# Kernel optimization log

Measured on AMD Instinct MI355X. Metric: run time of the kernel, lower is better.

The kernel has to match this reference:

```python
import jax, jax.numpy as jnp
import numpy as np

# ---------------- Chu-Liu-Edmonds MST decode (faithful numpy port) ----------------

def _find_cycle(parents, length, current_nodes):
    added = [False] * length
    added[0] = True
    cycle = set()
    has_cycle = False
    for i in range(1, length):
        if has_cycle:
            break
        if added[i] or not current_nodes[i]:
            continue
        this_cycle = {i}
        added[i] = True
        has_cycle = True
        next_node = i
        while parents[next_node] not in this_cycle:
            next_node = parents[next_node]
            if added[next_node]:
                has_cycle = False
                break
            added[next_node] = True
            this_cycle.add(next_node)
        if has_cycle:
            original = next_node
            cycle.add(original)
            next_node = parents[original]
            while next_node != original:
                cycle.add(next_node)
                next_node = parents[next_node]
            break
    return has_cycle, list(cycle)


def chu_liu_edmonds(length, score_matrix, current_nodes, final_edges, old_input, old_output, representatives):
    parents = [-1]
    for node1 in range(1, length):
        parents.append(0)
        if current_nodes[node1]:
            max_score = score_matrix[0, node1]
            for node2 in range(1, length):
                if node2 == node1 or not current_nodes[node2]:
                    continue
                new_score = score_matrix[node2, node1]
                if new_score > max_score:
                    max_score = new_score
                    parents[node1] = node2
    has_cycle, cycle = _find_cycle(parents, length, current_nodes)
    if not has_cycle:
        final_edges[0] = -1
        for node in range(1, length):
            if not current_nodes[node]:
                continue
            parent = old_input[parents[node], node]
            child = old_output[parents[node], node]
            final_edges[child] = parent
        return
    cycle_weight = 0.0
    for node in cycle:
        cycle_weight += score_matrix[parents[node], node]
    cycle_representative = cycle[0]
    for node in range(length):
        if not current_nodes[node] or node in cycle:
            continue
        in_edge_weight = float('-inf')
        in_edge = -1
        out_edge_weight = float('-inf')
        out_edge = -1
        for node_in_cycle in cycle:
            if score_matrix[node_in_cycle, node] > in_edge_weight:
                in_edge_weight = score_matrix[node_in_cycle, node]
                in_edge = node_in_cycle
            score = cycle_weight + score_matrix[node, node_in_cycle] - score_matrix[parents[node_in_cycle], node_in_cycle]
            if score > out_edge_weight:
                out_edge_weight = score
                out_edge = node_in_cycle
        score_matrix[cycle_representative, node] = in_edge_weight
        old_input[cycle_representative, node] = old_input[in_edge, node]
        old_output[cycle_representative, node] = old_output[in_edge, node]
        score_matrix[node, cycle_representative] = out_edge_weight
        old_output[node, cycle_representative] = old_output[node, out_edge]
        old_input[node, cycle_representative] = old_input[node, out_edge]
    considered = []
    for i, node_in_cycle in enumerate(cycle):
        considered.append(set())
        if i > 0:
            current_nodes[node_in_cycle] = False
        for node in representatives[node_in_cycle]:
            considered[i].add(node)
            if i > 0:
                representatives[cycle_representative].add(node)
    chu_liu_edmonds(length, score_matrix, current_nodes, final_edges, old_input, old_output, representatives)
    found = False
    key_node = -1
    for i, node in enumerate(cycle):
        for cycle_rep in considered[i]:
            if cycle_rep in final_edges:
                key_node = node
                found = True
                break
        if found:
            break
    previous = parents[key_node]
    while previous != key_node:
        child = old_output[parents[previous], previous]
        parent = old_input[parents[previous], previous]
        final_edges[child] = parent
        previous = parents[previous]


def decode_mst(energy, length):
    # energy: numpy [num_labels, T, T]
    max_length = energy.shape[-1]
    energy = energy[:, :length, :length]
    label_id_matrix = energy.argmax(axis=0)
    score_matrix = np.array(energy.max(axis=0), copy=True)
    old_input = np.zeros([length, length], dtype=np.int32)
    old_output = np.zeros([length, length], dtype=np.int32)
    current_nodes = [True] * length
    representatives = []
    for node1 in range(length):
        score_matrix[node1, node1] = 0.0
        representatives.append({node1})
        for node2 in range(node1 + 1, length):
            old_input[node1, node2] = node1
            old_output[node1, node2] = node2
            old_input[node2, node1] = node2
            old_output[node2, node1] = node1
    final_edges = {}
    chu_liu_edmonds(length, score_matrix, current_nodes, final_edges, old_input, old_output, representatives)
    heads = np.zeros([max_length], np.int32)
    head_type = np.ones([max_length], np.int32)
    for child, parent in final_edges.items():
        heads[child] = parent
        head_type[child] = label_id_matrix[parent, child]
    return heads, head_type


# ---------------- biaffine scoring (jax) ----------------

@jax.jit
def _energy(encoded_text, W_head_arc, b_head_arc, W_dep_arc, b_dep_arc, U_arc,
            W_head_lab, b_head_lab, W_dep_lab, b_dep_lab, U_lab):
    h_arc = jax.nn.elu(encoded_text @ W_head_arc + b_head_arc)   # [B,T,A]
    d_arc = jax.nn.elu(encoded_text @ W_dep_arc + b_dep_arc)     # [B,T,A]
    arc_scores = jnp.einsum('bia,ac,bjc->bij', h_arc, U_arc, d_arc)  # head i -> dep j
    h_lab = jax.nn.elu(encoded_text @ W_head_lab + b_head_lab)   # [B,T,R]
    d_lab = jax.nn.elu(encoded_text @ W_dep_lab + b_dep_lab)     # [B,T,R]
    lab_scores = jnp.einsum('bir,lrs,bjs->blij', h_lab, U_lab, d_lab)  # [B,L,T,T]
    norm_arc = jax.nn.log_softmax(arc_scores, axis=1)   # normalize over heads
    norm_lab = jax.nn.log_softmax(lab_scores, axis=1)   # normalize over labels
    return jnp.exp(norm_arc[:, None, :, :] + norm_lab)  # [B,L,T,T] edge energies


def setup_inputs() -> dict:
    key = jax.random.key(0)
    ks = jax.random.split(key, 8)
    B, T, D, A, R, L = 32, 128, 768, 512, 128, 50
    s = 0.02
    return {
        'encoded_text': jax.random.normal(ks[0], (B, T, D), jnp.float32),
        'W_head_arc': jax.random.normal(ks[1], (D, A), jnp.float32) * s,
        'b_head_arc': jnp.zeros((A,), jnp.float32),
        'W_dep_arc': jax.random.normal(ks[2], (D, A), jnp.float32) * s,
        'b_dep_arc': jnp.zeros((A,), jnp.float32),
        'U_arc': jax.random.normal(ks[3], (A, A), jnp.float32) * s,
        'W_head_lab': jax.random.normal(ks[4], (D, R), jnp.float32) * s,
        'b_head_lab': jnp.zeros((R,), jnp.float32),
        'W_dep_lab': jax.random.normal(ks[5], (D, R), jnp.float32) * s,
        'b_dep_lab': jnp.zeros((R,), jnp.float32),
        'U_lab': jax.random.normal(ks[6], (L, R, R), jnp.float32) * s,
        'mask': jnp.ones((B, T), jnp.bool_),
    }


def reference(encoded_text, W_head_arc, b_head_arc, W_dep_arc, b_dep_arc, U_arc,
              W_head_lab, b_head_lab, W_dep_lab, b_dep_lab, U_lab, mask):
    energy = _energy(encoded_text, W_head_arc, b_head_arc, W_dep_arc, b_dep_arc, U_arc,
                     W_head_lab, b_head_lab, W_dep_lab, b_dep_lab, U_lab)
    lengths = np.asarray(mask.sum(-1))
    energy_np = np.asarray(energy)
    heads, tags = [], []
    # per-example Chu-Liu-Edmonds decode (inherently sequential, as in the original)
    for i in range(energy_np.shape[0]):
        h, t = decode_mst(energy_np[i], int(lengths[i]))
        heads.append(h)
        tags.append(t)
    return energy, jnp.asarray(np.stack(heads)), jnp.asarray(np.stack(tags))
```

## Files before the change

### kernel.cpp

```cpp
#include <hip/hip_runtime.h>
#include <math.h>

#define B_ 32
#define T_ 128
#define D_ 768
#define A_ 512
#define R_ 128
#define L_ 50

__global__ __launch_bounds__(256)
void proj_gemm_k(const float* __restrict__ X,
                 const float* __restrict__ Wha, const float* __restrict__ bha,
                 const float* __restrict__ Wda, const float* __restrict__ bda,
                 const float* __restrict__ Whl, const float* __restrict__ bhl,
                 const float* __restrict__ Wdl, const float* __restrict__ bdl,
                 float* __restrict__ HA, float* __restrict__ DA,
                 float* __restrict__ HL, float* __restrict__ DL)
{
    __shared__ float As[16][68];
    __shared__ float Bs[16][132];
    const int bx = blockIdx.x;
    const float *W, *bias; float* C; int ld, ncol;
    if (bx < 4)      { W = Wha; bias = bha; C = HA; ld = 512; ncol = bx * 128; }
    else if (bx < 8) { W = Wda; bias = bda; C = DA; ld = 512; ncol = (bx - 4) * 128; }
    else if (bx == 8){ W = Whl; bias = bhl; C = HL; ld = 128; ncol = 0; }
    else             { W = Wdl; bias = bdl; C = DL; ld = 128; ncol = 0; }
    const int m0 = blockIdx.y * 64;
    const int tid = threadIdx.x;
    const int tx = tid & 15, ry = tid >> 4;
    float acc[4][8] = {};
    for (int k0 = 0; k0 < 768; k0 += 16) {
        {
            int row = tid >> 2, kb = (tid & 3) * 4;
            float4 a = *(const float4*)&X[(size_t)(m0 + row) * 768 + k0 + kb];
            As[kb + 0][row] = a.x; As[kb + 1][row] = a.y;
            As[kb + 2][row] = a.z; As[kb + 3][row] = a.w;
        }
        {
            int kk = tid >> 4, c0 = (tid & 15) * 4;
            const float* Bp = &W[(size_t)(k0 + kk) * ld + ncol + c0];
            *(float4*)&Bs[kk][c0] = *(const float4*)&Bp[0];
            *(float4*)&Bs[kk][c0 + 64] = *(const float4*)&Bp[64];
        }
        __syncthreads();
#pragma unroll
        for (int kk = 0; kk < 16; ++kk) {
            float4 a4 = *(const float4*)&As[kk][ry * 4];
            float4 b0 = *(const float4*)&Bs[kk][tx * 4];
            float4 b1 = *(const float4*)&Bs[kk][tx * 4 + 64];
            float av[4] = { a4.x, a4.y, a4.z, a4.w };
            float bv[8] = { b0.x, b0.y, b0.z, b0.w, b1.x, b1.y, b1.z, b1.w };
#pragma unroll
            for (int i = 0; i < 4; ++i)
#pragma unroll
                for (int j = 0; j < 8; ++j)
                    acc[i][j] += av[i] * bv[j];
        }
        __syncthreads();
    }
    float bv0[8];
    {
        float4 q0 = *(const float4*)&bias[ncol + tx * 4];
        float4 q1 = *(const float4*)&bias[ncol + tx * 4 + 64];
        bv0[0] = q0.x; bv0[1] = q0.y; bv0[2] = q0.z; bv0[3] = q0.w;
        bv0[4] = q1.x; bv0[5] = q1.y; bv0[6] = q1.z; bv0[7] = q1.w;
    }
#pragma unroll
    for (int i = 0; i < 4; ++i) {
        int m = m0 + ry * 4 + i;
        size_t base = (size_t)m * ld + ncol;
        float o[8];
#pragma unroll
        for (int j = 0; j < 8; ++j) {
            float v = acc[i][j] + bv0[j];
            o[j] = v > 0.0f ? v : expm1f(v);
        }
        float4 s0 = { o[0], o[1], o[2], o[3] };
        float4 s1 = { o[4], o[5], o[6], o[7] };
        *(float4*)&C[base + tx * 4] = s0;
        *(float4*)&C[base + tx * 4 + 64] = s1;
    }
}

__global__ __launch_bounds__(256)
void gemm_k(const float* __restrict__ A, const float* __restrict__ B,
            const float* __restrict__ bias, float* __restrict__ C,
            int K, int lda, int ldb, int ldc,
            long long sA, long long sB, long long sC, long long c_outer, int flags)
{
    __shared__ float As[16][68];
    __shared__ float Bs[16][132];
    A += (size_t)blockIdx.z * sA;
    B += (size_t)blockIdx.z * sB;
    C += (size_t)blockIdx.z * sC;
    const int m0 = blockIdx.y * 64, n0 = blockIdx.x * 128;
    const int tid = threadIdx.x;
    const int tx = tid & 15, ry = tid >> 4;
    float acc[4][8] = {};
    for (int k0 = 0; k0 < K; k0 += 16) {
        {
            int row = tid >> 2, kb = (tid & 3) * 4;
            float4 a = *(const float4*)&A[(size_t)(m0 + row) * lda + k0 + kb];
            As[kb + 0][row] = a.x; As[kb + 1][row] = a.y;
            As[kb + 2][row] = a.z; As[kb + 3][row] = a.w;
        }
        if (!(flags & 4)) {
            int kk = tid >> 4, c0 = (tid & 15) * 4;
            const float* Bp = &B[(size_t)(k0 + kk) * ldb + n0 + c0];
            *(float4*)&Bs[kk][c0] = *(const float4*)&Bp[0];
            *(float4*)&Bs[kk][c0 + 64] = *(const float4*)&Bp[64];
        } else {
            int col = tid >> 1, kb = (tid & 1) * 8;
            const float* Bp = &B[(size_t)(n0 + col) * ldb + k0 + kb];
            float4 b0 = *(const float4*)&Bp[0];
            float4 b1 = *(const float4*)&Bp[4];
            Bs[kb + 0][col] = b0.x; Bs[kb + 1][col] = b0.y;
            Bs[kb + 2][col] = b0.z; Bs[kb + 3][col] = b0.w;
            Bs[kb + 4][col] = b1.x; Bs[kb + 5][col] = b1.y;
            Bs[kb + 6][col] = b1.z; Bs[kb + 7][col] = b1.w;
        }
        __syncthreads();
#pragma unroll
        for (int kk = 0; kk < 16; ++kk) {
            float4 a4 = *(const float4*)&As[kk][ry * 4];
            float4 b0 = *(const float4*)&Bs[kk][tx * 4];
            float4 b1 = *(const float4*)&Bs[kk][tx * 4 + 64];
            float av[4] = { a4.x, a4.y, a4.z, a4.w };
            float bv[8] = { b0.x, b0.y, b0.z, b0.w, b1.x, b1.y, b1.z, b1.w };
#pragma unroll
            for (int i = 0; i < 4; ++i)
#pragma unroll
                for (int j = 0; j < 8; ++j)
                    acc[i][j] += av[i] * bv[j];
        }
        __syncthreads();
    }
    float bv0[8] = {};
    if (flags & 1) {
        float4 q0 = *(const float4*)&bias[n0 + tx * 4];
        float4 q1 = *(const float4*)&bias[n0 + tx * 4 + 64];
        bv0[0] = q0.x; bv0[1] = q0.y; bv0[2] = q0.z; bv0[3] = q0.w;
        bv0[4] = q1.x; bv0[5] = q1.y; bv0[6] = q1.z; bv0[7] = q1.w;
    }
#pragma unroll
    for (int i = 0; i < 4; ++i) {
        int m = m0 + ry * 4 + i;
        size_t base = (size_t)(m >> 7) * c_outer + (size_t)(m & 127) * ldc + n0;
        float o[8];
#pragma unroll
        for (int j = 0; j < 8; ++j) {
            float v = acc[i][j] + bv0[j];
            if (flags & 2) v = v > 0.0f ? v : expm1f(v);
            o[j] = v;
        }
        float4 s0 = { o[0], o[1], o[2], o[3] };
        float4 s1 = { o[4], o[5], o[6], o[7] };
        *(float4*)&C[base + tx * 4] = s0;
        *(float4*)&C[base + tx * 4 + 64] = s1;
    }
}

__global__ __launch_bounds__(256)
void transpose_k(const float* __restrict__ in, float* __restrict__ out)
{
    __shared__ float tile[32][33];
    int b = blockIdx.z;
    int bx = blockIdx.x, by = blockIdx.y;
    int tx = threadIdx.x, ty = threadIdx.y;
    const float* src = in + (size_t)b * T_ * R_;
    float* dst = out + (size_t)b * T_ * R_;
#pragma unroll
    for (int r = 0; r < 4; ++r)
        tile[ty + 8 * r][tx] = src[(size_t)(by * 32 + ty + 8 * r) * 128 + bx * 32 + tx];
    __syncthreads();
#pragma unroll
    for (int r = 0; r < 4; ++r)
        dst[(size_t)(bx * 32 + ty + 8 * r) * 128 + by * 32 + tx] = tile[tx][ty + 8 * r];
}

__global__ __launch_bounds__(128)
void arc_logsoftmax_k(float* __restrict__ arc)
{
    int b = blockIdx.x, j = threadIdx.x;
    float* base = arc + (size_t)b * T_ * T_ + j;
    float m = -INFINITY;
    for (int i = 0; i < T_; ++i) m = fmaxf(m, base[(size_t)i * T_]);
    float s = 0.0f;
    for (int i = 0; i < T_; ++i) s += expf(base[(size_t)i * T_] - m);
    float ls = m + logf(s);
    for (int i = 0; i < T_; ++i) base[(size_t)i * T_] -= ls;
}

__global__ __launch_bounds__(256)
void lab_inplace_k(float* __restrict__ E, const float* __restrict__ dlt)
{
    __shared__ __align__(16) float As[T_ * R_];
    int l = blockIdx.x, b = blockIdx.y;
    float* base = E + ((size_t)b * L_ + l) * T_ * T_;
    int tid = threadIdx.x;
#pragma unroll
    for (int it = 0; it < 16; ++it) {
        int idx = (it * 256 + tid) * 4;
        *(float4*)&As[idx] = *(const float4*)&base[idx];
    }
    __syncthreads();
    int tx = tid & 15, ty = tid >> 4;
    int j0 = tx * 8, i0 = ty * 8;
    const float* dl = dlt + (size_t)b * T_ * R_;
    float acc[8][8] = {};
    for (int s0 = 0; s0 < R_; s0 += 4) {
        float a[8][4], bb[4][8];
#pragma unroll
        for (int ii = 0; ii < 8; ++ii) {
            float4 v = *(const float4*)&As[(i0 + ii) * R_ + s0];
            a[ii][0] = v.x; a[ii][1] = v.y; a[ii][2] = v.z; a[ii][3] = v.w;
        }
#pragma unroll
        for (int ss = 0; ss < 4; ++ss) {
            float4 x = *(const float4*)&dl[(size_t)(s0 + ss) * T_ + j0];
            float4 y = *(const float4*)&dl[(size_t)(s0 + ss) * T_ + j0 + 4];
            bb[ss][0] = x.x; bb[ss][1] = x.y; bb[ss][2] = x.z; bb[ss][3] = x.w;
            bb[ss][4] = y.x; bb[ss][5] = y.y; bb[ss][6] = y.z; bb[ss][7] = y.w;
        }
#pragma unroll
        for (int ii = 0; ii < 8; ++ii)
#pragma unroll
            for (int jj = 0; jj < 8; ++jj)
#pragma unroll
                for (int ss = 0; ss < 4; ++ss)
                    acc[ii][jj] += a[ii][ss] * bb[ss][jj];
    }
#pragma unroll
    for (int ii = 0; ii < 8; ++ii) {
        float4 o0 = { acc[ii][0], acc[ii][1], acc[ii][2], acc[ii][3] };
        float4 o1 = { acc[ii][4], acc[ii][5], acc[ii][6], acc[ii][7] };
        *(float4*)&base[(size_t)(i0 + ii) * T_ + j0] = o0;
        *(float4*)&base[(size_t)(i0 + ii) * T_ + j0 + 4] = o1;
    }
}

__global__ __launch_bounds__(256)
void energy_combine_k(float* __restrict__ E, const float* __restrict__ narc,
                      float* __restrict__ score_g, unsigned char* __restrict__ labmax_g)
{
    int g = blockIdx.x * 256 + threadIdx.x;
    int b = g >> 14;
    int ij = g & 16383;
    float* base = E + (size_t)b * L_ * T_ * T_ + ij;
    float v[L_];
    float m = -INFINITY;
    int am = 0;
#pragma unroll
    for (int l = 0; l < L_; ++l) {
        v[l] = base[(size_t)l * T_ * T_];
        if (v[l] > m) { m = v[l]; am = l; }
    }
    float s = 0.0f;
#pragma unroll
    for (int l = 0; l < L_; ++l) s += expf(v[l] - m);
    float ls = m + logf(s);
    float na = narc[(size_t)b * T_ * T_ + ij];
#pragma unroll
    for (int l = 0; l < L_; ++l) base[(size_t)l * T_ * T_] = expf(na + v[l] - ls);
    int i = ij >> 7, j = ij & 127;
    score_g[(size_t)b * 16384 + ij] = (i == j) ? 0.0f : expf(na + m - ls);
    labmax_g[(size_t)b * 16384 + ij] = (unsigned char)am;
}

__global__ __launch_bounds__(256)
void mst_k(const float* __restrict__ score_g, const unsigned char* __restrict__ labmax_g,
           float* __restrict__ heads, float* __restrict__ tags,
           unsigned char* __restrict__ pst_ws, unsigned char* __restrict__ tst_ws,
           unsigned char* __restrict__ cst_ws)
{
    int b = blockIdx.x, t = threadIdx.x;
    __shared__ float score[128 * 128];
    __shared__ unsigned char oin[128 * 128];
    __shared__ unsigned char oout[128 * 128];
    __shared__ int parents[128];
    __shared__ int fe[128];
    __shared__ float pmx[128];
    __shared__ int pp[128];
    __shared__ float sub[128];
    __shared__ unsigned char curr[128], cyc[128], cycidx[128], oncyc[128], pstrow[128];
    __shared__ int key_sh;

    volatile float* vscore = score;
    volatile int* vpar = parents;
    volatile int* vfe = fe;
    volatile unsigned char* vcurr = curr;
    volatile unsigned char* vcyc = cyc;
    volatile unsigned char* vcycidx = cycidx;
    volatile unsigned char* voncyc = oncyc;
    volatile unsigned char* voin = oin;
    volatile unsigned char* voout = oout;
    volatile unsigned char* vpstrow = pstrow;
    volatile float* vsub = sub;

    unsigned char* pst = pst_ws + (size_t)b * 16384;
    unsigned char* tst = tst_ws + (size_t)b * 16384;
    unsigned char* cst = cst_ws + (size_t)b * 16384;

    {
        const float4* src = (const float4*)(score_g + (size_t)b * 16384);
#pragma unroll
        for (int r = 0; r < 16; ++r)
            ((float4*)score)[r * 256 + t] = src[r * 256 + t];
    }
    {
        int row = t >> 1, half = t & 1;
        unsigned int tv = (unsigned int)row * 0x01010101u;
        unsigned int* oinw = (unsigned int*)&oin[row * 128];
        unsigned int* ooutw = (unsigned int*)&oout[row * 128];
#pragma unroll
        for (int w = 0; w < 16; ++w) {
            int idx = half * 16 + w;
            oinw[idx] = tv;
            ooutw[idx] = 0x03020100u + 0x04040404u * (unsigned int)idx;
        }
    }
    if (t < 128) { fe[t] = -2; curr[t] = 1; }
    __syncthreads();
    if (t < 128) {
        score[t * 128 + t] = -INFINITY;
        oin[t * 129] = 0; oout[t * 129] = 0;
    }
    __syncthreads();
    float mxl = 0.0f; int pl = 0;
    if (t >= 128) {
        int col = t - 128;
        float mx = -INFINITY; int pu = 64;
        if (col != 0) {
            mx = score[64 * 128 + col];
#pragma unroll 16
            for (int n2 = 65; n2 < 128; ++n2) {
                float sc = score[n2 * 128 + col];
                if (sc > mx) { mx = sc; pu = n2; }
            }
        }
        pmx[col] = mx; pp[col] = pu;
    } else if (t != 0) {
        mxl = score[t]; pl = 0;
#pragma unroll 16
        for (int n2 = 1; n2 < 64; ++n2) {
            float sc = score[n2 * 128 + t];
            if (sc > mxl) { mxl = sc; pl = n2; }
        }
    }
    __syncthreads();
    if (t == 0) parents[0] = -1;
    else if (t < 128) parents[t] = (pmx[t] > mxl) ? pp[t] : pl;
    __syncthreads();

    if (t < 64) {
        const int n0 = t, n1 = t + 64;
        int p0 = vpar[n0], p1 = vpar[n1];
        int c0 = 1, c1 = 1;
        int r0 = n0, r1 = n1;
        int lev = 0;
        for (;;) {
            int a0 = (n0 == 0 || !c0) ? 0 : p0;
            int a1 = (!c1) ? 0 : p1;
            int m0 = n0, m1 = n1;
#pragma unroll
            for (int s = 0; s < 7; ++s) {
                int src0 = a0 & 63, sel0 = a0 & 64;
                int src1 = a1 & 63, sel1 = a1 & 64;
                int g00 = __shfl(a0, src0, 64);
                int g01 = __shfl(a1, src0, 64);
                int h00 = __shfl(m0, src0, 64);
                int h01 = __shfl(m1, src0, 64);
                int g10 = __shfl(a0, src1, 64);
                int g11 = __shfl(a1, src1, 64);
                int h10 = __shfl(m0, src1, 64);
                int h11 = __shfl(m1, src1, 64);
                int na0 = sel0 ? g01 : g00;
                int nm0 = sel0 ? h01 : h00;
                int na1 = sel1 ? g11 : g10;
                int nm1 = sel1 ? h11 : h10;
                m0 = nm0 < m0 ? nm0 : m0;
                m1 = nm1 < m1 ? nm1 : m1;
                a0 = na0; a1 = na1;
            }
            int pred0 = (n0 >= 1) && c0 && (a0 != 0);
            int pred1 = c1 && (a1 != 0);
            unsigned long long bal0 = __ballot(pred0);
            unsigned long long bal1 = __ballot(pred1);
            if (bal0 == 0ull && bal1 == 0ull) {
                if (n0 == 0) vfe[0] = -1;
                else if (c0) {
                    int pa = voin[p0 * 128 + n0];
                    int ch = voout[p0 * 128 + n0];
                    vfe[ch] = pa;
                }
                if (c1) {
                    int pa = voin[p1 * 128 + n1];
                    int ch = voout[p1 * 128 + n1];
                    vfe[ch] = pa;
                }
                __threadfence_block();
                break;
            }
            voncyc[n0] = 0; voncyc[n1] = 0;
            __threadfence_block();
            if (pred0) voncyc[a0] = 1;
            if (pred1) voncyc[a1] = 1;
            __threadfence_block();
            int onc0 = voncyc[n0], onc1 = voncyc[n1];
            int cand0 = onc0 ? n0 : 255;
            int cand1 = onc1 ? n1 : 255;
            int cand = cand1 < cand0 ? cand1 : cand0;
#pragma unroll
            for (int off = 32; off >= 1; off >>= 1) {
                int oc = __shfl_xor(cand, off, 64);
                cand = oc < cand ? oc : cand;
            }
            const int rep = cand;
            int member0 = onc0 && (m0 == rep);
            int member1 = onc1 && (m1 == rep);
            unsigned long long mb0 = __ballot(member0);
            unsigned long long mb1 = __ballot(member1);
            int clen = __popcll(mb0) + __popcll(mb1);
            int rank0 = (int)__popcll(mb0 & ((1ull << n0) - 1ull));
            int rank1 = (int)__popcll(mb0) + (int)__popcll(mb1 & ((1ull << t) - 1ull));
            float s0m = 0.0f, s1m = 0.0f;
            if (member0) s0m = vscore[p0 * 128 + n0];
            if (member1) s1m = vscore[p1 * 128 + n1];
            float cw = s0m + s1m;
#pragma unroll
            for (int off = 32; off >= 1; off >>= 1)
                cw += __shfl_xor(cw, off, 64);
            vcycidx[n0] = member0 ? (unsigned char)rank0 : (unsigned char)0xFF;
            vcycidx[n1] = member1 ? (unsigned char)rank1 : (unsigned char)0xFF;
            if (member0) { vcyc[rank0] = (unsigned char)n0; vsub[rank0] = s0m;
                           cst[lev * 128 + rank0] = (unsigned char)n0; }
            if (member1) { vcyc[rank1] = (unsigned char)n1; vsub[rank1] = s1m;
                           cst[lev * 128 + rank1] = (unsigned char)n1; }
            __threadfence_block();
            pst[lev * 128 + n0] = (unsigned char)p0;
            pst[lev * 128 + n1] = (unsigned char)p1;
            int tg0 = vcycidx[r0], tg1 = vcycidx[r1];
            tst[lev * 128 + n0] = (unsigned char)tg0;
            tst[lev * 128 + n1] = (unsigned char)tg1;
#pragma unroll
            for (int half = 0; half < 2; ++half) {
                int n = half ? n1 : n0;
                int cc = half ? c1 : c0;
                int mem = half ? member1 : member0;
                if (cc && !mem) {
                    float inw = -INFINITY, outw = -INFINITY;
                    int ine = 0, oute = 0;
                    for (int i = 0; i < clen; ++i) {
                        int nic = (int)vcyc[i];
                        float sb = vsub[i];
                        float si = vscore[nic * 128 + n];
                        if (si > inw) { inw = si; ine = nic; }
                        float so = cw + vscore[n * 128 + nic] - sb;
                        if (so > outw) { outw = so; oute = nic; }
                    }
                    vscore[rep * 128 + n] = inw;
                    voin[rep * 128 + n] = voin[ine * 128 + n];
                    voout[rep * 128 + n] = voout[ine * 128 + n];
                    vscore[n * 128 + rep] = outw;
                    voout[n * 128 + rep] = voout[n * 128 + oute];
                    voin[n * 128 + rep] = voin[n * 128 + oute];
                }
            }
            __threadfence_block();
            if (member0 && n0 != rep) { c0 = 0; vcurr[n0] = 0; }
            if (member1 && n1 != rep) { c1 = 0; vcurr[n1] = 0; }
            if (tg0 != 0xFF) r0 = rep;
            if (tg1 != 0xFF) r1 = rep;
            if (c0 && n0 != 0 && n0 != rep && vcycidx[p0] != 0xFF) p0 = rep;
            if (c1 && n1 != rep && vcycidx[p1] != 0xFF) p1 = rep;
            {
                float cv0 = c0 ? vscore[n0 * 128 + rep] : -INFINITY;
                float cv1 = c1 ? vscore[n1 * 128 + rep] : -INFINITY;
                float bv; int bi;
                if (cv1 > cv0) { bv = cv1; bi = n1; } else { bv = cv0; bi = n0; }
#pragma unroll
                for (int off = 32; off >= 1; off >>= 1) {
                    float ov = __shfl_xor(bv, off, 64);
                    int oi = __shfl_xor(bi, off, 64);
                    if (ov > bv || (ov == bv && oi < bi)) { bv = ov; bi = oi; }
                }
                if (n0 == rep) p0 = bi;
                if (n1 == rep) p1 = bi;
            }
            vpar[n0] = p0; vpar[n1] = p1;
            __threadfence_block();
            ++lev;
        }
        for (int l2 = lev - 1; l2 >= 0; --l2) {
            int q0 = pst[l2 * 128 + n0], q1 = pst[l2 * 128 + n1];
            vpstrow[n0] = (unsigned char)q0;
            vpstrow[n1] = (unsigned char)q1;
            int tg0 = tst[l2 * 128 + n0], tg1 = tst[l2 * 128 + n1];
            __threadfence_block();
            if (tg0 != 0xFF && vfe[n0] != -2) *(volatile int*)&key_sh = (int)cst[l2 * 128 + tg0];
            if (tg1 != 0xFF && vfe[n1] != -2) *(volatile int*)&key_sh = (int)cst[l2 * 128 + tg1];
            __threadfence_block();
            if (t == 0) {
                int key = *(volatile int*)&key_sh;
                int prev = (int)vpstrow[key];
                int guard = 0;
                while (prev != key && guard++ < 200) {
                    int pp2 = (int)vpstrow[prev];
                    int ch = (int)voout[pp2 * 128 + prev];
                    int pa = (int)voin[pp2 * 128 + prev];
                    vfe[ch] = pa;
                    prev = pp2;
                }
            }
            __threadfence_block();
        }
    }
    __syncthreads();

    if (t < 128) {
        int f = fe[t];
        float h, ht;
        if (f != -2) {
            h = (float)f;
            int prow = (f < 0) ? 127 : f;
            ht = (float)(int)labmax_g[(size_t)b * 16384 + prow * 128 + t];
        } else { h = 0.0f; ht = 1.0f; }
        heads[b * 128 + t] = h;
        tags[b * 128 + t] = ht;
    }
}

extern "C" void kernel_launch(void* const* d_in, const int* in_sizes, int n_in,
                              void* d_out, int out_size, void* d_ws, size_t ws_size,
                              hipStream_t stream)
{
    const float* X   = (const float*)d_in[0];
    const float* Wha = (const float*)d_in[1];
    const float* bha = (const float*)d_in[2];
    const float* Wda = (const float*)d_in[3];
    const float* bda = (const float*)d_in[4];
    const float* Ua  = (const float*)d_in[5];
    const float* Whl = (const float*)d_in[6];
    const float* bhl = (const float*)d_in[7];
    const float* Wdl = (const float*)d_in[8];
    const float* bdl = (const float*)d_in[9];
    const float* Ul  = (const float*)d_in[10];

    char* ws = (char*)d_ws;
    float* HA    = (float*)(ws + (size_t)0);
    float* DA    = (float*)(ws + ((size_t)8 << 20));
    float* TA    = (float*)(ws + ((size_t)16 << 20));
    float* HL    = (float*)(ws + ((size_t)24 << 20));
    float* DL    = (float*)(ws + ((size_t)26 << 20));
    float* DLt   = (float*)(ws + ((size_t)28 << 20));
    float* ARC   = (float*)(ws + ((size_t)30 << 20));
    float* SCORE = (float*)(ws + ((size_t)32 << 20));
    unsigned char* LABMAX = (unsigned char*)(ws + ((size_t)34 << 20));
    unsigned char* PST  = LABMAX + (size_t)32 * 16384;
    unsigned char* TST  = PST  + (size_t)32 * 16384;
    unsigned char* CST  = TST  + (size_t)32 * 16384;

    float* E     = (float*)d_out;
    float* heads = E + (size_t)B_ * L_ * T_ * T_;
    float* tags  = heads + (size_t)B_ * T_;

    dim3 thr(256);
    proj_gemm_k<<<dim3(10, 64), thr, 0, stream>>>(X, Wha, bha, Wda, bda, Whl, bhl, Wdl, bdl,
                                                  HA, DA, HL, DL);
    gemm_k<<<dim3(4, 64, 1), thr, 0, stream>>>(HA, Ua, nullptr, TA, 512, 512, 512, 512, 0, 0, 0, (long long)128 * 512, 0);
    transpose_k<<<dim3(4, 4, 32), dim3(32, 8), 0, stream>>>(DL, DLt);
    gemm_k<<<dim3(1, 2, 32), thr, 0, stream>>>(TA, DA, nullptr, ARC, 512, 512, 512, 128, 65536, 65536, 16384, 0, 4);
    arc_logsoftmax_k<<<32, 128, 0, stream>>>(ARC);
    gemm_k<<<dim3(1, 64, 50), thr, 0, stream>>>(HL, Ul, nullptr, E, 128, 128, 128, 128, 0, 16384, 16384, (long long)50 * 16384, 0);
    lab_inplace_k<<<dim3(50, 32), thr, 0, stream>>>(E, DLt);
    energy_combine_k<<<2048, 256, 0, stream>>>(E, ARC, SCORE, LABMAX);
    mst_k<<<32, 256, 0, stream>>>(SCORE, LABMAX, heads, tags, PST, TST, CST);
}
```

Baseline: 1.032 ms.

## Move MST contraction history to LDS and streamline cycle detection in wavefront

Moves the per-level contraction history arrays (parent, tag and cycle tables) out of global workspace and into shared memory. The pointer-jumping loop now packs parent and minimum into one word, halving the shuffles per round, and runs only as many rounds as the active node count needs. Cycle marking uses epoch-stamped bytes with a ballot instead of a clear pass and a shuffle reduction, and membership checks read ballot masks instead of a shared index array. Shared memory rises by 48 KB per block, and the cycle-weight sum is now a serial loop over the cycle length.

```diff
diff --git a/kernel.cpp b/kernel.cpp
--- a/kernel.cpp
+++ b/kernel.cpp
@@ -269,37 +269,34 @@
 
 __global__ __launch_bounds__(256)
 void mst_k(const float* __restrict__ score_g, const unsigned char* __restrict__ labmax_g,
-           float* __restrict__ heads, float* __restrict__ tags,
-           unsigned char* __restrict__ pst_ws, unsigned char* __restrict__ tst_ws,
-           unsigned char* __restrict__ cst_ws)
+           float* __restrict__ heads, float* __restrict__ tags)
 {
     int b = blockIdx.x, t = threadIdx.x;
     __shared__ float score[128 * 128];
     __shared__ unsigned char oin[128 * 128];
     __shared__ unsigned char oout[128 * 128];
+    __shared__ unsigned char pstL[128 * 128];
+    __shared__ unsigned char tstL[128 * 128];
+    __shared__ unsigned char cstL[128 * 128];
     __shared__ int parents[128];
     __shared__ int fe[128];
     __shared__ float pmx[128];
     __shared__ int pp[128];
     __shared__ float sub[128];
-    __shared__ unsigned char curr[128], cyc[128], cycidx[128], oncyc[128], pstrow[128];
-    __shared__ int key_sh;
+    __shared__ unsigned char cyc[128], oncyc[128], pstrow[128];
 
     volatile float* vscore = score;
     volatile int* vpar = parents;
     volatile int* vfe = fe;
-    volatile unsigned char* vcurr = curr;
     volatile unsigned char* vcyc = cyc;
-    volatile unsigned char* vcycidx = cycidx;
     volatile unsigned char* voncyc = oncyc;
     volatile unsigned char* voin = oin;
     volatile unsigned char* voout = oout;
     volatile unsigned char* vpstrow = pstrow;
     volatile float* vsub = sub;
-
-    unsigned char* pst = pst_ws + (size_t)b * 16384;
-    unsigned char* tst = tst_ws + (size_t)b * 16384;
-    unsigned char* cst = cst_ws + (size_t)b * 16384;
+    volatile unsigned char* vcst = cstL;
+    volatile unsigned char* vpst = pstL;
+    volatile unsigned char* vtst = tstL;
 
     {
         const float4* src = (const float4*)(score_g + (size_t)b * 16384);
@@ -319,7 +316,7 @@
             ooutw[idx] = 0x03020100u + 0x04040404u * (unsigned int)idx;
         }
     }
-    if (t < 128) { fe[t] = -2; curr[t] = 1; }
+    if (t < 128) { fe[t] = -2; oncyc[t] = 0; }
     __syncthreads();
     if (t < 128) {
         score[t * 128 + t] = -INFINITY;
@@ -358,29 +355,24 @@
         int c0 = 1, c1 = 1;
         int r0 = n0, r1 = n1;
         int lev = 0;
+        int nact = 128;
         for (;;) {
+            int rounds = 32 - __clz(nact - 1);
             int a0 = (n0 == 0 || !c0) ? 0 : p0;
             int a1 = (!c1) ? 0 : p1;
             int m0 = n0, m1 = n1;
-#pragma unroll
-            for (int s = 0; s < 7; ++s) {
-                int src0 = a0 & 63, sel0 = a0 & 64;
-                int src1 = a1 & 63, sel1 = a1 & 64;
-                int g00 = __shfl(a0, src0, 64);
-                int g01 = __shfl(a1, src0, 64);
-                int h00 = __shfl(m0, src0, 64);
-                int h01 = __shfl(m1, src0, 64);
-                int g10 = __shfl(a0, src1, 64);
-                int g11 = __shfl(a1, src1, 64);
-                int h10 = __shfl(m0, src1, 64);
-                int h11 = __shfl(m1, src1, 64);
-                int na0 = sel0 ? g01 : g00;
-                int nm0 = sel0 ? h01 : h00;
-                int na1 = sel1 ? g11 : g10;
-                int nm1 = sel1 ? h11 : h10;
-                m0 = nm0 < m0 ? nm0 : m0;
-                m1 = nm1 < m1 ? nm1 : m1;
-                a0 = na0; a1 = na1;
+            for (int s = 0; s < rounds; ++s) {
+                int pk0 = (a0 << 7) | m0;
+                int pk1 = (a1 << 7) | m1;
+                int s0l = a0 & 63, s1l = a1 & 63;
+                int q00 = __shfl(pk0, s0l, 64);
+                int q01 = __shfl(pk1, s0l, 64);
+                int q10 = __shfl(pk0, s1l, 64);
+                int q11 = __shfl(pk1, s1l, 64);
+                int g0 = (a0 & 64) ? q01 : q00;
+                int g1 = (a1 & 64) ? q11 : q10;
+                a0 = g0 >> 7; int gm0 = g0 & 127; m0 = gm0 < m0 ? gm0 : m0;
+                a1 = g1 >> 7; int gm1 = g1 & 127; m1 = gm1 < m1 ? gm1 : m1;
             }
             int pred0 = (n0 >= 1) && c0 && (a0 != 0);
             int pred1 = c1 && (a1 != 0);
@@ -401,47 +393,44 @@
                 __threadfence_block();
                 break;
             }
-            voncyc[n0] = 0; voncyc[n1] = 0;
+            unsigned char ep = (unsigned char)(lev + 1);
+            if (pred0) voncyc[a0] = ep;
+            if (pred1) voncyc[a1] = ep;
             __threadfence_block();
-            if (pred0) voncyc[a0] = 1;
-            if (pred1) voncyc[a1] = 1;
-            __threadfence_block();
-            int onc0 = voncyc[n0], onc1 = voncyc[n1];
-            int cand0 = onc0 ? n0 : 255;
-            int cand1 = onc1 ? n1 : 255;
-            int cand = cand1 < cand0 ? cand1 : cand0;
-#pragma unroll
-            for (int off = 32; off >= 1; off >>= 1) {
-                int oc = __shfl_xor(cand, off, 64);
-                cand = oc < cand ? oc : cand;
-            }
-            const int rep = cand;
+            int onc0 = (voncyc[n0] == ep);
+            int onc1 = (voncyc[n1] == ep);
+            unsigned long long ob0 = __ballot(onc0);
+            unsigned long long ob1 = __ballot(onc1);
+            const int rep = ob0 ? ((int)__ffsll((long long)ob0) - 1)
+                                : (64 + (int)__ffsll((long long)ob1) - 1);
             int member0 = onc0 && (m0 == rep);
             int member1 = onc1 && (m1 == rep);
             unsigned long long mb0 = __ballot(member0);
             unsigned long long mb1 = __ballot(member1);
-            int clen = __popcll(mb0) + __popcll(mb1);
+            int clen = (int)__popcll(mb0) + (int)__popcll(mb1);
             int rank0 = (int)__popcll(mb0 & ((1ull << n0) - 1ull));
-            int rank1 = (int)__popcll(mb0) + (int)__popcll(mb1 & ((1ull << t) - 1ull));
-            float s0m = 0.0f, s1m = 0.0f;
-            if (member0) s0m = vscore[p0 * 128 + n0];
-            if (member1) s1m = vscore[p1 * 128 + n1];
-            float cw = s0m + s1m;
-#pragma unroll
-            for (int off = 32; off >= 1; off >>= 1)
-                cw += __shfl_xor(cw, off, 64);
-            vcycidx[n0] = member0 ? (unsigned char)rank0 : (unsigned char)0xFF;
-            vcycidx[n1] = member1 ? (unsigned char)rank1 : (unsigned char)0xFF;
+            int rank1 = (int)__popcll(mb0) + (int)__popcll(mb1 & ((1ull << n0) - 1ull));
+            float s0m = member0 ? vscore[p0 * 128 + n0] : 0.0f;
+            float s1m = member1 ? vscore[p1 * 128 + n1] : 0.0f;
             if (member0) { vcyc[rank0] = (unsigned char)n0; vsub[rank0] = s0m;
-                           cst[lev * 128 + rank0] = (unsigned char)n0; }
+                           vcst[lev * 128 + rank0] = (unsigned char)n0; }
             if (member1) { vcyc[rank1] = (unsigned char)n1; vsub[rank1] = s1m;
-                           cst[lev * 128 + rank1] = (unsigned char)n1; }
+                           vcst[lev * 128 + rank1] = (unsigned char)n1; }
+            vpst[lev * 128 + n0] = (unsigned char)p0;
+            vpst[lev * 128 + n1] = (unsigned char)p1;
+            int mbit_r0 = (r0 < 64) ? (int)((mb0 >> r0) & 1ull) : (int)((mb1 >> (r0 - 64)) & 1ull);
+            int mbit_r1 = (r1 < 64) ? (int)((mb0 >> r1) & 1ull) : (int)((mb1 >> (r1 - 64)) & 1ull);
+            int tg0 = mbit_r0 ? ((r0 < 64) ? (int)__popcll(mb0 & ((1ull << r0) - 1ull))
+                                           : (int)__popcll(mb0) + (int)__popcll(mb1 & ((1ull << (r0 - 64)) - 1ull)))
+                              : 0xFF;
+            int tg1 = mbit_r1 ? ((r1 < 64) ? (int)__popcll(mb0 & ((1ull << r1) - 1ull))
+                                           : (int)__popcll(mb0) + (int)__popcll(mb1 & ((1ull << (r1 - 64)) - 1ull)))
+                              : 0xFF;
+            vtst[lev * 128 + n0] = (unsigned char)tg0;
+            vtst[lev * 128 + n1] = (unsigned char)tg1;
             __threadfence_block();
-            pst[lev * 128 + n0] = (unsigned char)p0;
-            pst[lev * 128 + n1] = (unsigned char)p1;
-            int tg0 = vcycidx[r0], tg1 = vcycidx[r1];
-            tst[lev * 128 + n0] = (unsigned char)tg0;
-            tst[lev * 128 + n1] = (unsigned char)tg1;
+            float cw = 0.0f;
+            for (int i = 0; i < clen; ++i) cw += vsub[i];
 #pragma unroll
             for (int half = 0; half < 2; ++half) {
                 int n = half ? n1 : n0;
@@ -467,12 +456,14 @@
                 }
             }
             __threadfence_block();
-            if (member0 && n0 != rep) { c0 = 0; vcurr[n0] = 0; }
-            if (member1 && n1 != rep) { c1 = 0; vcurr[n1] = 0; }
+            if (member0 && n0 != rep) c0 = 0;
+            if (member1 && n1 != rep) c1 = 0;
             if (tg0 != 0xFF) r0 = rep;
             if (tg1 != 0xFF) r1 = rep;
-            if (c0 && n0 != 0 && n0 != rep && vcycidx[p0] != 0xFF) p0 = rep;
-            if (c1 && n1 != rep && vcycidx[p1] != 0xFF) p1 = rep;
+            int mbit_p0 = (p0 < 64) ? (int)((mb0 >> p0) & 1ull) : (int)((mb1 >> (p0 - 64)) & 1ull);
+            int mbit_p1 = (p1 < 64) ? (int)((mb0 >> p1) & 1ull) : (int)((mb1 >> (p1 - 64)) & 1ull);
+            if (c0 && n0 != 0 && n0 != rep && mbit_p0) p0 = rep;
+            if (c1 && n1 != rep && mbit_p1) p1 = rep;
             {
                 float cv0 = c0 ? vscore[n0 * 128 + rep] : -INFINITY;
                 float cv1 = c1 ? vscore[n1 * 128 + rep] : -INFINITY;
@@ -487,21 +478,25 @@
                 if (n0 == rep) p0 = bi;
                 if (n1 == rep) p1 = bi;
             }
-            vpar[n0] = p0; vpar[n1] = p1;
-            __threadfence_block();
+            nact -= (clen - 1);
             ++lev;
         }
         for (int l2 = lev - 1; l2 >= 0; --l2) {
-            int q0 = pst[l2 * 128 + n0], q1 = pst[l2 * 128 + n1];
+            int q0 = vpst[l2 * 128 + n0], q1 = vpst[l2 * 128 + n1];
             vpstrow[n0] = (unsigned char)q0;
             vpstrow[n1] = (unsigned char)q1;
-            int tg0 = tst[l2 * 128 + n0], tg1 = tst[l2 * 128 + n1];
+            int tg0 = vtst[l2 * 128 + n0], tg1 = vtst[l2 * 128 + n1];
+            int kf0 = (tg0 != 0xFF) && (vfe[n0] != -2);
+            int kf1 = (tg1 != 0xFF) && (vfe[n1] != -2);
+            int kv0 = kf0 ? (int)vcst[l2 * 128 + tg0] : 0;
+            int kv1 = kf1 ? (int)vcst[l2 * 128 + tg1] : 0;
+            unsigned long long kb0 = __ballot(kf0);
+            unsigned long long kb1 = __ballot(kf1);
+            int key = -1;
+            if (kb0)      key = __shfl(kv0, (int)__ffsll((long long)kb0) - 1, 64);
+            else if (kb1) key = __shfl(kv1, (int)__ffsll((long long)kb1) - 1, 64);
             __threadfence_block();
-            if (tg0 != 0xFF && vfe[n0] != -2) *(volatile int*)&key_sh = (int)cst[l2 * 128 + tg0];
-            if (tg1 != 0xFF && vfe[n1] != -2) *(volatile int*)&key_sh = (int)cst[l2 * 128 + tg1];
-            __threadfence_block();
-            if (t == 0) {
-                int key = *(volatile int*)&key_sh;
+            if (t == 0 && key >= 0) {
                 int prev = (int)vpstrow[key];
                 int guard = 0;
                 while (prev != key && guard++ < 200) {
@@ -556,9 +551,6 @@
     float* ARC   = (float*)(ws + ((size_t)30 << 20));
     float* SCORE = (float*)(ws + ((size_t)32 << 20));
     unsigned char* LABMAX = (unsigned char*)(ws + ((size_t)34 << 20));
-    unsigned char* PST  = LABMAX + (size_t)32 * 16384;
-    unsigned char* TST  = PST  + (size_t)32 * 16384;
-    unsigned char* CST  = TST  + (size_t)32 * 16384;
 
     float* E     = (float*)d_out;
     float* heads = E + (size_t)B_ * L_ * T_ * T_;
@@ -574,5 +566,5 @@
     gemm_k<<<dim3(1, 64, 50), thr, 0, stream>>>(HL, Ul, nullptr, E, 128, 128, 128, 128, 0, 16384, 16384, (long long)50 * 16384, 0);
     lab_inplace_k<<<dim3(50, 32), thr, 0, stream>>>(E, DLt);
     energy_combine_k<<<2048, 256, 0, stream>>>(E, ARC, SCORE, LABMAX);
-    mst_k<<<32, 256, 0, stream>>>(SCORE, LABMAX, heads, tags, PST, TST, CST);
-}
+    mst_k<<<32, 256, 0, stream>>>(SCORE, LABMAX, heads, tags);
+}
```

New measurement: 942.5 us. -8.7%, faster.
